# Kernel optimization log

Measured on AMD Instinct MI355X. Metric: run time of the kernel, lower is better.

## Reference

```python
import jax, jax.numpy as jnp
import numpy as np

TEMP = 0.07
EPS = 1e-12  # matches torch F.normalize default eps


def _l2norm(x):
    n = jnp.sqrt(jnp.sum(x * x, axis=-1, keepdims=True))
    return x / jnp.maximum(n, EPS)


def setup_inputs() -> dict:
    key = jax.random.key(0)
    kq, kk = jax.random.split(key)
    N, D = 16384, 256
    q = jax.random.normal(kq, (N, D), dtype=jnp.float32)
    k = jax.random.normal(kk, (N, D), dtype=jnp.float32)
    return {"q": q, "k": k}


def reference(q, k):
    qn = _l2norm(q)
    kn = _l2norm(k)
    logits = (qn @ kn.T) / TEMP            # [N, N]
    # cross-entropy with labels = arange(N): mean over rows of (logsumexp - diag)
    lse = jax.nn.logsumexp(logits, axis=-1)  # [N]
    diag = jnp.diagonal(logits)              # [N]
    return jnp.mean(lse - diag)
```

## Files before the change

kernel.cpp:

```cpp
#include <hip/hip_runtime.h>
#include <hip/hip_bf16.h>
#include <cstdint>
#include <cstddef>

#define NROWS 16384
#define DDIM  256
#define SPLITS 16
#define NTILES 256
#define TILES_PER (NTILES / SPLITS)

typedef __attribute__((ext_vector_type(4))) float f32x4;
typedef __attribute__((ext_vector_type(4))) float fl4;
typedef __attribute__((ext_vector_type(4))) int   i32x4;
typedef __attribute__((ext_vector_type(8))) int   i32x8;

constexpr float SCALE_EXP2 = 20.609929155556627f;
constexpr float LN2F       = 0.69314718055994531f;
constexpr float INV_T      = 14.285714285714286f;

__device__ inline void gload_lds16(const void* g, void* l) {
  __builtin_amdgcn_global_load_lds(
      (const __attribute__((address_space(1))) void*)g,
      (__attribute__((address_space(3))) void*)l, 16, 0, 0);
}

__global__ __launch_bounds__(256) void norm_kernel(
    const float* __restrict__ q, const float* __restrict__ k,
    unsigned char* __restrict__ qn, unsigned char* __restrict__ kn,
    float* __restrict__ diag, float* __restrict__ rowsum,
    float* __restrict__ out)
{
  const int wave = threadIdx.x >> 6, lane = threadIdx.x & 63;
  const int row = blockIdx.x * 4 + wave;
  const size_t off = (size_t)row * DDIM + lane * 4;

  fl4 vq = *(const fl4*)(q + off);
  fl4 vk = *(const fl4*)(k + off);
  float ssq = vq.x * vq.x + vq.y * vq.y + vq.z * vq.z + vq.w * vq.w;
  float ssk = vk.x * vk.x + vk.y * vk.y + vk.z * vk.z + vk.w * vk.w;
  float dot = vq.x * vk.x + vq.y * vk.y + vq.z * vk.z + vq.w * vk.w;
#pragma unroll
  for (int m = 1; m < 64; m <<= 1) {
    ssq += __shfl_xor(ssq, m, 64);
    ssk += __shfl_xor(ssk, m, 64);
    dot += __shfl_xor(dot, m, 64);
  }
  float rq = 1.0f / fmaxf(sqrtf(ssq), 1e-12f);
  float rk = 1.0f / fmaxf(sqrtf(ssk), 1e-12f);

  float sq = rq * SCALE_EXP2;
  int pq = __builtin_amdgcn_cvt_pk_fp8_f32(vq.x * sq, vq.y * sq, 0, false);
  pq     = __builtin_amdgcn_cvt_pk_fp8_f32(vq.z * sq, vq.w * sq, pq, true);
  *(int*)(qn + off) = pq;
  int pk = __builtin_amdgcn_cvt_pk_fp8_f32(vk.x * rk, vk.y * rk, 0, false);
  pk     = __builtin_amdgcn_cvt_pk_fp8_f32(vk.z * rk, vk.w * rk, pk, true);
  *(int*)(kn + off) = pk;

  if (lane == 0) {
    diag[row]   = dot * rq * rk * INV_T;
    rowsum[row] = 0.0f;
    if (row == 0) out[0] = 0.0f;
  }
}

__global__ __launch_bounds__(256) void lse_kernel(
    const unsigned char* __restrict__ qn, const unsigned char* __restrict__ kn,
    float* __restrict__ rowsum)
{
  __shared__ __attribute__((aligned(16))) unsigned char Bs[2][64 * DDIM];

  const int tid  = threadIdx.x;
  const int wave = tid >> 6, lane = tid & 63;
  const int l15  = lane & 15, quad = lane >> 4;
  const int split = blockIdx.x % SPLITS;
  const int rb    = blockIdx.x / SPLITS;
  const int wrow  = rb * 128 + wave * 32;
  const int t0 = split * TILES_PER;
  const int t1 = t0 + TILES_PER;

  const int Ln = tid >> 4, Ljj = tid & 15;
  const int Lj = Ljj ^ Ln;
  const size_t src_off = (size_t)Ln * DDIM + (size_t)Lj * 16;

  i32x8 A00, A01, A10, A11;
  {
    const unsigned char* ap0 = qn + (size_t)(wrow + l15) * DDIM + quad * 32;
    const unsigned char* ap1 = qn + (size_t)(wrow + 16 + l15) * DDIM + quad * 32;
    A00 = *(const i32x8*)(ap0);
    A01 = *(const i32x8*)(ap0 + 128);
    A10 = *(const i32x8*)(ap1);
    A11 = *(const i32x8*)(ap1 + 128);
  }

  const int rowoff = l15 * DDIM;
  const int c0  = quad * 2;
  const int o00 = rowoff + (((c0    ) ^ l15) * 16);
  const int o01 = rowoff + (((c0 + 1) ^ l15) * 16);
  const int o10 = rowoff + (((c0 + 8) ^ l15) * 16);
  const int o11 = rowoff + (((c0 + 9) ^ l15) * 16);

  f32x4 sums0 = {0.f, 0.f, 0.f, 0.f}, sums1 = {0.f, 0.f, 0.f, 0.f};
  f32x4 accE0, accE1, accO0, accO1;
  accO0 = (f32x4){-1e30f, -1e30f, -1e30f, -1e30f};
  accO1 = accO0;

  {
    const unsigned char* kbase = kn + (size_t)t0 * (64 * DDIM) + src_off;
#pragma unroll
    for (int i = 0; i < 4; ++i)
      gload_lds16(kbase + i * 4096, (void*)(Bs[0] + tid * 16 + i * 4096));
  }

#define EPI(P0, P1) do {                                                      \
    f32x4 e0_, e1_;                                                           \
    e0_[0] = __builtin_amdgcn_exp2f(P0[0]);                                   \
    e0_[1] = __builtin_amdgcn_exp2f(P0[1]);                                   \
    e0_[2] = __builtin_amdgcn_exp2f(P0[2]);                                   \
    e0_[3] = __builtin_amdgcn_exp2f(P0[3]);                                   \
    e1_[0] = __builtin_amdgcn_exp2f(P1[0]);                                   \
    e1_[1] = __builtin_amdgcn_exp2f(P1[1]);                                   \
    e1_[2] = __builtin_amdgcn_exp2f(P1[2]);                                   \
    e1_[3] = __builtin_amdgcn_exp2f(P1[3]);                                   \
    sums0 += e0_;                                                             \
    sums1 += e1_;                                                             \
  } while (0)

#define CS_STEP(C0, C1, P0, P1, BOFF) do {                                    \
    i32x4 lo0_ = *(const i32x4*)(bb + (BOFF) + o00);                          \
    i32x4 hi0_ = *(const i32x4*)(bb + (BOFF) + o01);                          \
    i32x4 lo1_ = *(const i32x4*)(bb + (BOFF) + o10);                          \
    i32x4 hi1_ = *(const i32x4*)(bb + (BOFF) + o11);                          \
    EPI(P0, P1);                  \
    i32x8 b0_ = {lo0_.x, lo0_.y, lo0_.z, lo0_.w, hi0_.x, hi0_.y, hi0_.z, hi0_.w}; \
    i32x8 b1_ = {lo1_.x, lo1_.y, lo1_.z, lo1_.w, hi1_.x, hi1_.y, hi1_.z, hi1_.w}; \
    __builtin_amdgcn_s_setprio(1);                                            \
    C0 = __builtin_amdgcn_mfma_scale_f32_16x16x128_f8f6f4(                    \
        A00, b0_, (f32x4){0.f, 0.f, 0.f, 0.f}, 0, 0, 0, 127, 0, 127);         \
    C1 = __builtin_amdgcn_mfma_scale_f32_16x16x128_f8f6f4(                    \
        A10, b0_, (f32x4){0.f, 0.f, 0.f, 0.f}, 0, 0, 0, 127, 0, 127);         \
    C0 = __builtin_amdgcn_mfma_scale_f32_16x16x128_f8f6f4(                    \
        A01, b1_, C0, 0, 0, 0, 127, 0, 127);                                  \
    C1 = __builtin_amdgcn_mfma_scale_f32_16x16x128_f8f6f4(                    \
        A11, b1_, C1, 0, 0, 0, 127, 0, 127);                                  \
    __builtin_amdgcn_s_setprio(0);                                            \
  } while (0)

  for (int ct = t0; ct < t1; ++ct) {
    const int cur = (ct - t0) & 1;
    __builtin_amdgcn_s_waitcnt(0x0F70);
    __syncthreads();
    if (ct + 1 < t1) {
      const unsigned char* kbase = kn + (size_t)(ct + 1) * (64 * DDIM) + src_off;
#pragma unroll
      for (int i = 0; i < 4; ++i)
        gload_lds16(kbase + i * 4096, (void*)(Bs[cur ^ 1] + tid * 16 + i * 4096));
    }
    const unsigned char* bb = Bs[cur];
    CS_STEP(accE0, accE1, accO0, accO1, 0);
    CS_STEP(accO0, accO1, accE0, accE1, 4096);
    CS_STEP(accE0, accE1, accO0, accO1, 8192);
    CS_STEP(accO0, accO1, accE0, accE1, 12288);
  }
  EPI(accO0, accO1);

#undef CS_STEP
#undef EPI

#pragma unroll
  for (int r = 0; r < 4; ++r) {
    float v0 = sums0[r], v1 = sums1[r];
    v0 += __shfl_xor(v0, 1, 64);  v1 += __shfl_xor(v1, 1, 64);
    v0 += __shfl_xor(v0, 2, 64);  v1 += __shfl_xor(v1, 2, 64);
    v0 += __shfl_xor(v0, 4, 64);  v1 += __shfl_xor(v1, 4, 64);
    v0 += __shfl_xor(v0, 8, 64);  v1 += __shfl_xor(v1, 8, 64);
    if (l15 == 0) {
      atomicAdd(&rowsum[wrow + quad * 4 + r], v0);
      atomicAdd(&rowsum[wrow + 16 + quad * 4 + r], v1);
    }
  }
}

__global__ void final_kernel(const float* __restrict__ rowsum,
                             const float* __restrict__ diag,
                             float* __restrict__ out)
{
  int row = blockIdx.x * 256 + threadIdx.x;
  float c = __builtin_amdgcn_logf(rowsum[row]) * LN2F - diag[row];
#pragma unroll
  for (int m = 1; m < 64; m <<= 1) c += __shfl_xor(c, m, 64);
  __shared__ float red[4];
  int wave = threadIdx.x >> 6, lane = threadIdx.x & 63;
  if (lane == 0) red[wave] = c;
  __syncthreads();
  if (threadIdx.x == 0) {
    float s = red[0] + red[1] + red[2] + red[3];
    atomicAdd(out, s * (1.0f / NROWS));
  }
}

extern "C" void kernel_launch(void* const* d_in, const int* in_sizes, int n_in,
                              void* d_out, int out_size, void* d_ws, size_t ws_size,
                              hipStream_t stream)
{
  const float* q = (const float*)d_in[0];
  const float* k = (const float*)d_in[1];
  float* out = (float*)d_out;

  char* ws = (char*)d_ws;
  unsigned char* qn = (unsigned char*)ws;
  unsigned char* kn = (unsigned char*)(ws + (4u << 20));
  float* diag   = (float*)(ws + (8u << 20));
  float* rowsum = (float*)(ws + (8u << 20) + (64u << 10));

  norm_kernel <<<NROWS / 4, 256, 0, stream>>>(q, k, qn, kn, diag, rowsum, out);
  lse_kernel  <<<(NROWS / 128) * SPLITS, 256, 0, stream>>>(qn, kn, rowsum);
  final_kernel<<<NROWS / 256, 256, 0, stream>>>(rowsum, diag, out);
}
```

Measured before the change: 142.8 us.

## Retile LSE waves into a 2x2 grid with 64 rows and half K-tile columns

Each wave now covers 64 query rows and half of the 64-column K tile (a 2x2 wave grid), instead of 32 rows and the full tile. Each B fragment read from LDS now feeds four MFMAs instead of two, halving LDS read traffic per MFMA. The cost is twice as many A-fragment and accumulator registers per wave, which may lower occupancy. The number of atomic adds per block also grows, because two waves now contribute to the same rows.

```diff
diff --git a/kernel.cpp b/kernel.cpp
--- a/kernel.cpp
+++ b/kernel.cpp
@@ -72,9 +72,10 @@
   const int tid  = threadIdx.x;
   const int wave = tid >> 6, lane = tid & 63;
   const int l15  = lane & 15, quad = lane >> 4;
+  const int wr   = wave >> 1, wc = wave & 1;
   const int split = blockIdx.x % SPLITS;
   const int rb    = blockIdx.x / SPLITS;
-  const int wrow  = rb * 128 + wave * 32;
+  const int wrow  = rb * 128 + wr * 64;
   const int t0 = split * TILES_PER;
   const int t1 = t0 + TILES_PER;
 
@@ -82,14 +83,16 @@
   const int Lj = Ljj ^ Ln;
   const size_t src_off = (size_t)Ln * DDIM + (size_t)Lj * 16;
 
-  i32x8 A00, A01, A10, A11;
+  i32x8 A00, A01, A10, A11, A20, A21, A30, A31;
   {
-    const unsigned char* ap0 = qn + (size_t)(wrow + l15) * DDIM + quad * 32;
+    const unsigned char* ap0 = qn + (size_t)(wrow      + l15) * DDIM + quad * 32;
     const unsigned char* ap1 = qn + (size_t)(wrow + 16 + l15) * DDIM + quad * 32;
-    A00 = *(const i32x8*)(ap0);
-    A01 = *(const i32x8*)(ap0 + 128);
-    A10 = *(const i32x8*)(ap1);
-    A11 = *(const i32x8*)(ap1 + 128);
+    const unsigned char* ap2 = qn + (size_t)(wrow + 32 + l15) * DDIM + quad * 32;
+    const unsigned char* ap3 = qn + (size_t)(wrow + 48 + l15) * DDIM + quad * 32;
+    A00 = *(const i32x8*)(ap0);  A01 = *(const i32x8*)(ap0 + 128);
+    A10 = *(const i32x8*)(ap1);  A11 = *(const i32x8*)(ap1 + 128);
+    A20 = *(const i32x8*)(ap2);  A21 = *(const i32x8*)(ap2 + 128);
+    A30 = *(const i32x8*)(ap3);  A31 = *(const i32x8*)(ap3 + 128);
   }
 
   const int rowoff = l15 * DDIM;
@@ -98,11 +101,13 @@
   const int o01 = rowoff + (((c0 + 1) ^ l15) * 16);
   const int o10 = rowoff + (((c0 + 8) ^ l15) * 16);
   const int o11 = rowoff + (((c0 + 9) ^ l15) * 16);
-
-  f32x4 sums0 = {0.f, 0.f, 0.f, 0.f}, sums1 = {0.f, 0.f, 0.f, 0.f};
-  f32x4 accE0, accE1, accO0, accO1;
+  const int cb0 = wc * 8192;
+
+  f32x4 sums0 = {0.f,0.f,0.f,0.f}, sums1 = {0.f,0.f,0.f,0.f};
+  f32x4 sums2 = {0.f,0.f,0.f,0.f}, sums3 = {0.f,0.f,0.f,0.f};
+  f32x4 accE0, accE1, accE2, accE3, accO0, accO1, accO2, accO3;
   accO0 = (f32x4){-1e30f, -1e30f, -1e30f, -1e30f};
-  accO1 = accO0;
+  accO1 = accO0; accO2 = accO0; accO3 = accO0;
 
   {
     const unsigned char* kbase = kn + (size_t)t0 * (64 * DDIM) + src_off;
@@ -111,37 +116,45 @@
       gload_lds16(kbase + i * 4096, (void*)(Bs[0] + tid * 16 + i * 4096));
   }
 
-#define EPI(P0, P1) do {                                                      \
-    f32x4 e0_, e1_;                                                           \
-    e0_[0] = __builtin_amdgcn_exp2f(P0[0]);                                   \
-    e0_[1] = __builtin_amdgcn_exp2f(P0[1]);                                   \
-    e0_[2] = __builtin_amdgcn_exp2f(P0[2]);                                   \
-    e0_[3] = __builtin_amdgcn_exp2f(P0[3]);                                   \
-    e1_[0] = __builtin_amdgcn_exp2f(P1[0]);                                   \
-    e1_[1] = __builtin_amdgcn_exp2f(P1[1]);                                   \
-    e1_[2] = __builtin_amdgcn_exp2f(P1[2]);                                   \
-    e1_[3] = __builtin_amdgcn_exp2f(P1[3]);                                   \
-    sums0 += e0_;                                                             \
-    sums1 += e1_;                                                             \
-  } while (0)
-
-#define CS_STEP(C0, C1, P0, P1, BOFF) do {                                    \
+#define EPI1(Pv, Sv) do {                                                     \
+    f32x4 e_;                                                                 \
+    e_[0] = __builtin_amdgcn_exp2f(Pv[0]);                                    \
+    e_[1] = __builtin_amdgcn_exp2f(Pv[1]);                                    \
+    e_[2] = __builtin_amdgcn_exp2f(Pv[2]);                                    \
+    e_[3] = __builtin_amdgcn_exp2f(Pv[3]);                                    \
+    Sv += e_;                                                                 \
+  } while (0)
+
+#define EPI(P) do {                                                           \
+    EPI1(P##0, sums0); EPI1(P##1, sums1);                                     \
+    EPI1(P##2, sums2); EPI1(P##3, sums3);                                     \
+  } while (0)
+
+#define CS_STEP(C, P, BOFF) do {                                              \
     i32x4 lo0_ = *(const i32x4*)(bb + (BOFF) + o00);                          \
     i32x4 hi0_ = *(const i32x4*)(bb + (BOFF) + o01);                          \
     i32x4 lo1_ = *(const i32x4*)(bb + (BOFF) + o10);                          \
     i32x4 hi1_ = *(const i32x4*)(bb + (BOFF) + o11);                          \
-    EPI(P0, P1);                  \
+    EPI(P);                \
     i32x8 b0_ = {lo0_.x, lo0_.y, lo0_.z, lo0_.w, hi0_.x, hi0_.y, hi0_.z, hi0_.w}; \
     i32x8 b1_ = {lo1_.x, lo1_.y, lo1_.z, lo1_.w, hi1_.x, hi1_.y, hi1_.z, hi1_.w}; \
     __builtin_amdgcn_s_setprio(1);                                            \
-    C0 = __builtin_amdgcn_mfma_scale_f32_16x16x128_f8f6f4(                    \
+    C##0 = __builtin_amdgcn_mfma_scale_f32_16x16x128_f8f6f4(                  \
         A00, b0_, (f32x4){0.f, 0.f, 0.f, 0.f}, 0, 0, 0, 127, 0, 127);         \
-    C1 = __builtin_amdgcn_mfma_scale_f32_16x16x128_f8f6f4(                    \
+    C##1 = __builtin_amdgcn_mfma_scale_f32_16x16x128_f8f6f4(                  \
         A10, b0_, (f32x4){0.f, 0.f, 0.f, 0.f}, 0, 0, 0, 127, 0, 127);         \
-    C0 = __builtin_amdgcn_mfma_scale_f32_16x16x128_f8f6f4(                    \
-        A01, b1_, C0, 0, 0, 0, 127, 0, 127);                                  \
-    C1 = __builtin_amdgcn_mfma_scale_f32_16x16x128_f8f6f4(                    \
-        A11, b1_, C1, 0, 0, 0, 127, 0, 127);                                  \
+    C##2 = __builtin_amdgcn_mfma_scale_f32_16x16x128_f8f6f4(                  \
+        A20, b0_, (f32x4){0.f, 0.f, 0.f, 0.f}, 0, 0, 0, 127, 0, 127);         \
+    C##3 = __builtin_amdgcn_mfma_scale_f32_16x16x128_f8f6f4(                  \
+        A30, b0_, (f32x4){0.f, 0.f, 0.f, 0.f}, 0, 0, 0, 127, 0, 127);         \
+    C##0 = __builtin_amdgcn_mfma_scale_f32_16x16x128_f8f6f4(                  \
+        A01, b1_, C##0, 0, 0, 0, 127, 0, 127);                                \
+    C##1 = __builtin_amdgcn_mfma_scale_f32_16x16x128_f8f6f4(                  \
+        A11, b1_, C##1, 0, 0, 0, 127, 0, 127);                                \
+    C##2 = __builtin_amdgcn_mfma_scale_f32_16x16x128_f8f6f4(                  \
+        A21, b1_, C##2, 0, 0, 0, 127, 0, 127);                                \
+    C##3 = __builtin_amdgcn_mfma_scale_f32_16x16x128_f8f6f4(                  \
+        A31, b1_, C##3, 0, 0, 0, 127, 0, 127);                                \
     __builtin_amdgcn_s_setprio(0);                                            \
   } while (0)
 
@@ -156,28 +169,32 @@
         gload_lds16(kbase + i * 4096, (void*)(Bs[cur ^ 1] + tid * 16 + i * 4096));
     }
     const unsigned char* bb = Bs[cur];
-    CS_STEP(accE0, accE1, accO0, accO1, 0);
-    CS_STEP(accO0, accO1, accE0, accE1, 4096);
-    CS_STEP(accE0, accE1, accO0, accO1, 8192);
-    CS_STEP(accO0, accO1, accE0, accE1, 12288);
-  }
-  EPI(accO0, accO1);
+    CS_STEP(accE, accO, cb0);
+    CS_STEP(accO, accE, cb0 + 4096);
+  }
+  EPI(accO);
 
 #undef CS_STEP
 #undef EPI
-
-#pragma unroll
-  for (int r = 0; r < 4; ++r) {
-    float v0 = sums0[r], v1 = sums1[r];
-    v0 += __shfl_xor(v0, 1, 64);  v1 += __shfl_xor(v1, 1, 64);
-    v0 += __shfl_xor(v0, 2, 64);  v1 += __shfl_xor(v1, 2, 64);
-    v0 += __shfl_xor(v0, 4, 64);  v1 += __shfl_xor(v1, 4, 64);
-    v0 += __shfl_xor(v0, 8, 64);  v1 += __shfl_xor(v1, 8, 64);
-    if (l15 == 0) {
-      atomicAdd(&rowsum[wrow + quad * 4 + r], v0);
-      atomicAdd(&rowsum[wrow + 16 + quad * 4 + r], v1);
-    }
-  }
+#undef EPI1
+
+#define RED(Sv, SROW) do {                                                    \
+    _Pragma("unroll")                                                         \
+    for (int r = 0; r < 4; ++r) {                                             \
+      float v = Sv[r];                                                        \
+      v += __shfl_xor(v, 1, 64);                                              \
+      v += __shfl_xor(v, 2, 64);                                              \
+      v += __shfl_xor(v, 4, 64);                                              \
+      v += __shfl_xor(v, 8, 64);                                              \
+      if (l15 == 0) atomicAdd(&rowsum[(SROW) + quad * 4 + r], v);             \
+    }                                                                         \
+  } while (0)
+
+  RED(sums0, wrow);
+  RED(sums1, wrow + 16);
+  RED(sums2, wrow + 32);
+  RED(sums3, wrow + 48);
+#undef RED
 }
 
 __global__ void final_kernel(const float* __restrict__ rowsum,
```

Result: slower. 148.3 us (+3.9%).
